# Performance work log

Measured on AMD Instinct MI355X. Metric: run time of the kernel, lower is better.

The kernel has to match this reference:

```python
import jax, jax.numpy as jnp
import numpy as np

BETA = 0.25

def conv1d(x, w, b=None, stride=1, pad=0):
    # x: (B, C_in, T), w: (C_out, C_in, K)
    y = jax.lax.conv_general_dilated(x, w, (stride,), [(pad, pad)],
                                     dimension_numbers=('NCW', 'OIW', 'NCW'))
    if b is not None:
        y = y + b[None, :, None]
    return y

def setup_inputs() -> dict:
    key = jax.random.key(0)
    ks = jax.random.split(key, 16)
    B, C_in, T = 64, 64, 4096
    h, rh, D, K = 128, 64, 64, 512
    s = 0.05
    f32 = jnp.float32
    return {
        'x': jax.random.normal(ks[0], (B, C_in, T), f32),
        'w1': jax.random.normal(ks[1], (h // 2, C_in, 4), f32) * s,
        'b1': jnp.zeros((h // 2,), f32),
        'w2': jax.random.normal(ks[2], (h, h // 2, 4), f32) * s,
        'b2': jnp.zeros((h,), f32),
        'w3': jax.random.normal(ks[3], (h, h, 3), f32) * s,
        'b3': jnp.zeros((h,), f32),
        'res0_w1': jax.random.normal(ks[4], (rh, h, 3), f32) * s,
        'res0_w2': jax.random.normal(ks[5], (h, rh, 1), f32) * s,
        'res1_w1': jax.random.normal(ks[6], (rh, h, 3), f32) * s,
        'res1_w2': jax.random.normal(ks[7], (h, rh, 1), f32) * s,
        'w_out': jax.random.normal(ks[8], (D, h, 1), f32) * s,
        'b_out': jnp.zeros((D,), f32),
        'wpq': jax.random.normal(ks[9], (D, D, 1), f32) * s,
        'bpq': jnp.zeros((D,), f32),
        'codebook': jax.random.uniform(ks[10], (K, D), f32, -1.0 / K, 1.0 / K),
    }

def reference(x, w1, b1, w2, b2, w3, b3, res0_w1, res0_w2, res1_w1, res1_w2,
              w_out, b_out, wpq, bpq, codebook):
    # ---- Encoder (1D conv downsampling + residual stack) ----
    hcur = jax.nn.relu(conv1d(x, w1, b1, stride=2, pad=1))       # (B, h/2, T/2)
    hcur = jax.nn.relu(conv1d(hcur, w2, b2, stride=2, pad=1))    # (B, h, T/4)
    hcur = conv1d(hcur, w3, b3, stride=1, pad=1)                 # (B, h, T')
    for wa, wb in ((res0_w1, res0_w2), (res1_w1, res1_w2)):
        hcur = hcur + conv1d(jax.nn.relu(conv1d(jax.nn.relu(hcur), wa, None, 1, 1)), wb, None, 1, 0)
    hcur = jax.nn.relu(hcur)
    hcur = conv1d(hcur, w_out, b_out)                            # (B, D, T')
    # ---- pre-quantization 1x1 conv (module permutes to channel-first and back) ----
    z = conv1d(hcur, wpq, bpq)                                   # (B, D, T')
    z_e = jnp.transpose(z, (0, 2, 1))                            # (B, T', D)
    B, Tq, D = z_e.shape
    K = codebook.shape[0]
    # ---- Vector quantization ----
    flat = z_e.reshape(-1, D)                                    # (N, D)
    d = (jnp.sum(flat * flat, axis=1, keepdims=True)
         + jnp.sum(codebook * codebook, axis=1)[None, :]
         - 2.0 * flat @ codebook.T)                              # (N, K)
    idx = jnp.argmin(d, axis=1)                                  # (N,)
    encodings = jax.nn.one_hot(idx, K, dtype=z_e.dtype)          # (N, K)
    z_q = codebook[idx].reshape(B, Tq, D)                        # gather
    sg = jax.lax.stop_gradient
    embedding_loss = jnp.mean((sg(z_q) - z_e) ** 2) + BETA * jnp.mean((z_q - sg(z_e)) ** 2)
    z_q_st = z_e + sg(z_q - z_e)                                 # straight-through
    e_mean = jnp.mean(encodings, axis=0)
    perplexity = jnp.exp(-jnp.sum(e_mean * jnp.log(e_mean + 1e-10)))
    encoding_indices = idx.reshape(-1, 1)
    return (embedding_loss, z_q_st, perplexity, z_e, encodings, encoding_indices)
```

## Files before the change

### kernel.cpp

```cpp
#include <hip/hip_runtime.h>
#include <math.h>


typedef short short8 __attribute__((ext_vector_type(8)));
typedef float f32x4 __attribute__((ext_vector_type(4)));

__device__ __forceinline__ unsigned short bf16hi(float f) {
  unsigned u = __builtin_bit_cast(unsigned, f);
  return (unsigned short)((u + 0x7FFFu + ((u >> 16) & 1u)) >> 16);
}
__device__ __forceinline__ float bf16tof(unsigned short h) {
  unsigned u = ((unsigned)h) << 16;
  return __builtin_bit_cast(float, u);
}
__device__ __forceinline__ void split3(float f, unsigned short& h,
                                       unsigned short& m, unsigned short& l) {
  h = bf16hi(f);
  float r = f - bf16tof(h);
  m = bf16hi(r);
  l = bf16hi(r - bf16tof(m));
}

template<int CIN, int TAPS, int S, bool RELU_IN, bool HAS_BIAS, bool RESID,
         bool CHW_IN, bool OUT_NOGUARD>
__global__ __launch_bounds__(256) void conv_mfma(
    const float* __restrict__ in, const short* __restrict__ Ab,
    const float* __restrict__ bias, const float* __restrict__ resid,
    float* __restrict__ out, int Tin, int Tout, int MTG)
{
  constexpr int nCk   = CIN / 32;
  constexpr int RS    = (S == 2) ? 130 : ((TAPS == 3) ? 66 : 64);
  constexpr int ROWBS = 40;

  __shared__ short xhi[RS * ROWBS];
  __shared__ short xmd[RS * ROWBS];
  __shared__ short xlo[RS * ROWBS];

  const int tid  = threadIdx.x;
  const int lane = tid & 63;
  const int wv   = tid >> 6;
  const int ih   = wv & 1;
  const int jh   = wv >> 1;
  const int tl   = lane & 15;
  const int q    = lane >> 4;
  const int b    = blockIdx.y;
  const int t0   = blockIdx.x * 64;
  const int co0  = blockIdx.z * 64;
  const int COUT = MTG * 16;

  const int rbase = (S == 2) ? (2 * t0) : ((TAPS == 3) ? t0 : (t0 + 1));

  f32x4 acc[2][2] = {};

  for (int ch = 0; ch < nCk; ch++) {
    if (ch) __syncthreads();

    if constexpr (!CHW_IN) {
      for (int i = tid; i < RS * 8; i += 256) {
        int rl = i >> 3;
        int c4 = (i & 7) * 4;
        int rg = rbase + rl;
        const float* sp = in + ((size_t)b * (Tin + 2) + rg) * CIN + ch * 32 + c4;
        float4 v = *(const float4*)sp;
        if (RELU_IN) {
          v.x = fmaxf(v.x, 0.f); v.y = fmaxf(v.y, 0.f);
          v.z = fmaxf(v.z, 0.f); v.w = fmaxf(v.w, 0.f);
        }
        float vv[4] = {v.x, v.y, v.z, v.w};
        unsigned short h[4], m[4], l[4];
        #pragma unroll
        for (int e = 0; e < 4; e++) split3(vv[e], h[e], m[e], l[e]);
        int slot = (S == 2) ? ((rl & 1) * 65 + (rl >> 1)) : rl;
        int off = slot * ROWBS + c4;
        uint2 uh, um, ul;
        uh.x = (unsigned)h[0] | ((unsigned)h[1] << 16);
        uh.y = (unsigned)h[2] | ((unsigned)h[3] << 16);
        um.x = (unsigned)m[0] | ((unsigned)m[1] << 16);
        um.y = (unsigned)m[2] | ((unsigned)m[3] << 16);
        ul.x = (unsigned)l[0] | ((unsigned)l[1] << 16);
        ul.y = (unsigned)l[2] | ((unsigned)l[3] << 16);
        *(uint2*)(xhi + off) = uh;
        *(uint2*)(xmd + off) = um;
        *(uint2*)(xlo + off) = ul;
      }
    } else {
      if (tid < 32) {
        int cig = ch * 32 + tid;
        int tin = 2 * t0 - 1;
        float v = 0.f;
        if (tin >= 0) v = in[((size_t)b * 64 + cig) * Tin + tin];
        unsigned short h, m, l;
        split3(v, h, m, l);
        xhi[tid] = (short)h;
        xmd[tid] = (short)m;
        xlo[tid] = (short)l;
      }
      int cil = tid >> 3, tq = tid & 7;
      for (int base = tq * 4; base <= 128; base += 32) {
        int tin0 = 2 * t0 + base;
        const float* sp = in + ((size_t)b * 64 + ch * 32 + cil) * Tin + tin0;
        float vv[4];
        if (tin0 + 3 < Tin) {
          float4 t4 = *(const float4*)sp;
          vv[0] = t4.x; vv[1] = t4.y; vv[2] = t4.z; vv[3] = t4.w;
        } else {
          #pragma unroll
          for (int e = 0; e < 4; e++) vv[e] = (tin0 + e < Tin) ? sp[e] : 0.f;
        }
        #pragma unroll
        for (int e = 0; e < 4; e++) {
          int rl = base + e + 1;
          if (rl <= 129) {
            unsigned short h, m, l;
            split3(vv[e], h, m, l);
            int slot = (rl & 1) * 65 + (rl >> 1);
            xhi[slot * ROWBS + cil] = (short)h;
            xmd[slot * ROWBS + cil] = (short)m;
            xlo[slot * ROWBS + cil] = (short)l;
          }
        }
      }
    }
    __syncthreads();

    #pragma unroll
    for (int tap = 0; tap < TAPS; tap++) {
      short8 ah[2], am[2], al[2];
      #pragma unroll
      for (int mi = 0; mi < 2; mi++) {
        const short* ab = Ab +
            (size_t)(((ch * TAPS + tap) * MTG + (co0 >> 4) + ih * 2 + mi) * 3) * 512
            + lane * 8;
        ah[mi] = *(const short8*)ab;
        am[mi] = *(const short8*)(ab + 512);
        al[mi] = *(const short8*)(ab + 1024);
      }
      #pragma unroll
      for (int nt = 0; nt < 2; nt++) {
        int tpos = jh * 32 + nt * 16 + tl;
        int slot;
        if constexpr (S == 2)         slot = (tap & 1) * 65 + tpos + (tap >> 1);
        else if constexpr (TAPS == 3) slot = tpos + tap;
        else                          slot = tpos;
        const int xo = slot * ROWBS + q * 8;
        short8 bh = *(const short8*)(xhi + xo);
        short8 bm = *(const short8*)(xmd + xo);
        short8 bl = *(const short8*)(xlo + xo);
        #pragma unroll
        for (int mi = 0; mi < 2; mi++) {
          acc[mi][nt] = __builtin_amdgcn_mfma_f32_16x16x32_bf16(ah[mi], bh, acc[mi][nt], 0, 0, 0);
          acc[mi][nt] = __builtin_amdgcn_mfma_f32_16x16x32_bf16(ah[mi], bm, acc[mi][nt], 0, 0, 0);
          acc[mi][nt] = __builtin_amdgcn_mfma_f32_16x16x32_bf16(am[mi], bh, acc[mi][nt], 0, 0, 0);
          acc[mi][nt] = __builtin_amdgcn_mfma_f32_16x16x32_bf16(am[mi], bm, acc[mi][nt], 0, 0, 0);
          acc[mi][nt] = __builtin_amdgcn_mfma_f32_16x16x32_bf16(ah[mi], bl, acc[mi][nt], 0, 0, 0);
          acc[mi][nt] = __builtin_amdgcn_mfma_f32_16x16x32_bf16(al[mi], bh, acc[mi][nt], 0, 0, 0);
        }
      }
    }
  }

  #pragma unroll
  for (int mi = 0; mi < 2; mi++) {
    #pragma unroll
    for (int nt = 0; nt < 2; nt++) {
      int t  = t0 + jh * 32 + nt * 16 + tl;
      int co = co0 + (ih * 2 + mi) * 16 + q * 4;
      f32x4 a = acc[mi][nt];
      float4 v = {a[0], a[1], a[2], a[3]};
      if constexpr (HAS_BIAS) {
        float4 bb = *(const float4*)(bias + co);
        v.x += bb.x; v.y += bb.y; v.z += bb.z; v.w += bb.w;
      }
      if constexpr (RESID) {
        float4 rr = *(const float4*)(resid + ((size_t)b * (Tout + 2) + t + 1) * COUT + co);
        v.x += rr.x; v.y += rr.y; v.z += rr.z; v.w += rr.w;
      }
      float* op;
      if constexpr (OUT_NOGUARD) op = out + ((size_t)b * Tout + t) * COUT + co;
      else                       op = out + ((size_t)b * (Tout + 2) + t + 1) * COUT + co;
      *(float4*)op = v;
    }
  }
}

__global__ __launch_bounds__(256) void prep_small(
    const float* __restrict__ wout, const float* __restrict__ bout,
    const float* __restrict__ wpq, const float* __restrict__ bpq,
    const float* __restrict__ cb,
    float* __restrict__ Wc, float* __restrict__ bc, float* __restrict__ cnorm)
{
  const int tid = threadIdx.x;
  for (int i = tid; i < 64 * 128; i += 256) {
    int d = i >> 7, c = i & 127;
    float s = 0.f;
    for (int e = 0; e < 64; e++) s = fmaf(wpq[d * 64 + e], wout[e * 128 + c], s);
    Wc[i] = s;
  }
  for (int i = tid; i < 64; i += 256) {
    float s = bpq[i];
    for (int e = 0; e < 64; e++) s = fmaf(wpq[i * 64 + e], bout[e], s);
    bc[i] = s;
  }
  for (int k = tid; k < 512; k += 256) {
    float s = 0.f;
    for (int d = 0; d < 64; d++) { float c = cb[k * 64 + d]; s = fmaf(c, c, s); }
    cnorm[k] = s;
  }
}

__device__ __forceinline__ void buildA(const float* w, short* dst,
                                       int COUT, int CIN, int TAPS, int idx)
{
  int lane = idx & 63;
  int rest = idx >> 6;
  int hl   = rest % 3;  rest /= 3;
  int mtg  = rest % (COUT / 16); rest /= (COUT / 16);
  int tap  = rest % TAPS;
  int chunk = rest / TAPS;
  int co  = mtg * 16 + (lane & 15);
  int ci0 = chunk * 32 + (lane >> 4) * 8;
  short v[8];
  #pragma unroll
  for (int j = 0; j < 8; j++) {
    float f = w[((size_t)co * CIN + ci0 + j) * TAPS + tap];
    unsigned short h, m, l;
    h = bf16hi(f);
    float r = f - bf16tof(h);
    m = bf16hi(r);
    l = bf16hi(r - bf16tof(m));
    v[j] = (hl == 0) ? (short)h : ((hl == 1) ? (short)m : (short)l);
  }
  int MTG = COUT / 16;
  size_t o = ((((size_t)(chunk * TAPS + tap) * MTG + mtg) * 3 + hl) * 64 + lane) * 8;
  #pragma unroll
  for (int j = 0; j < 8; j++) dst[o + j] = v[j];
}

__global__ __launch_bounds__(256) void prep_w_all(
    const float* w1, const float* w2, const float* w3,
    const float* r0a, const float* r0b, const float* r1a, const float* r1b,
    const float* Wc,
    short* A1, short* A2, short* A3, short* A4, short* A5, short* A6,
    short* A7, short* A8)
{
  int g = blockIdx.x * 256 + threadIdx.x;
  if      (g < 6144)  buildA(w1,  A1, 64,  64,  4, g);
  else if (g < 18432) buildA(w2,  A2, 128, 64,  4, g - 6144);
  else if (g < 36864) buildA(w3,  A3, 128, 128, 3, g - 18432);
  else if (g < 46080) buildA(r0a, A4, 64,  128, 3, g - 36864);
  else if (g < 49152) buildA(r0b, A5, 128, 64,  1, g - 46080);
  else if (g < 58368) buildA(r1a, A6, 64,  128, 3, g - 49152);
  else if (g < 61440) buildA(r1b, A7, 128, 64,  1, g - 58368);
  else if (g < 64512) buildA(Wc,  A8, 64,  128, 1, g - 61440);
}

__global__ __launch_bounds__(256) void zero_guards(
    float* __restrict__ sA, float* __restrict__ sB1,
    float* __restrict__ sB2, float* __restrict__ sC)
{
  int gt = blockIdx.x * 256 + threadIdx.x;
  int NT = gridDim.x * 256;
  for (int i = gt; i < 64 * 2 * 64; i += NT) {
    int b = i >> 7, r = (i >> 6) & 1, c = i & 63;
    sA[((size_t)b * 2050 + r * 2049) * 64 + c] = 0.f;
  }
  for (int i = gt; i < 64 * 2 * 128; i += NT) {
    int b = i >> 8, r = (i >> 7) & 1, c = i & 127;
    size_t o = ((size_t)b * 1026 + r * 1025) * 128 + c;
    sB1[o] = 0.f; sB2[o] = 0.f;
  }
  for (int i = gt; i < 64 * 2 * 64; i += NT) {
    int b = i >> 7, r = (i >> 6) & 1, c = i & 63;
    sC[((size_t)b * 1026 + r * 1025) * 64 + c] = 0.f;
  }
}

__global__ __launch_bounds__(256) void vq_k(
    const float* __restrict__ ze, const float* __restrict__ cb,
    const float* __restrict__ cnorm,
    float* __restrict__ zq_out, float* __restrict__ enc,
    float* __restrict__ idx_out,
    int* __restrict__ counts, float* __restrict__ loss_accum)
{
  __shared__ float rv0[256], rv1[256];
  __shared__ int   ri0[256], ri1[256];
  __shared__ int   idx_s[128];
  __shared__ float ls[4];

  const int tid  = threadIdx.x;
  const int lane = tid & 63;
  const int wv   = tid >> 6;
  const int wvu  = __builtin_amdgcn_readfirstlane(wv);
  const int n0   = blockIdx.x * 128;

  float zr0[64], zr1[64];
  {
    const float* zp0 = ze + (size_t)(n0 + lane) * 64;
    const float* zp1 = ze + (size_t)(n0 + 64 + lane) * 64;
    #pragma unroll
    for (int j = 0; j < 32; j++) {
      float2 a = *(const float2*)(zp0 + 2 * j);
      float2 b = *(const float2*)(zp1 + 2 * j);
      zr0[2 * j] = a.x; zr0[2 * j + 1] = a.y;
      zr1[2 * j] = b.x; zr1[2 * j + 1] = b.y;
    }
  }

  float best0 = 3.4e38f, best1 = 3.4e38f;
  int   bi0 = 0, bi1 = 0;

  #pragma unroll 2
  for (int r = 0; r < 128; r++) {
    const int c = wvu * 128 + r;
    const float* crow = cb + (size_t)c * 64;
    float s00 = 0.f, s01 = 0.f, s02 = 0.f, s03 = 0.f;
    float s10 = 0.f, s11 = 0.f, s12 = 0.f, s13 = 0.f;
    #pragma unroll
    for (int d = 0; d < 64; d += 4) {
      float4 cv = *(const float4*)(crow + d);
      s00 = fmaf(cv.x, zr0[d],     s00);
      s01 = fmaf(cv.y, zr0[d + 1], s01);
      s02 = fmaf(cv.z, zr0[d + 2], s02);
      s03 = fmaf(cv.w, zr0[d + 3], s03);
      s10 = fmaf(cv.x, zr1[d],     s10);
      s11 = fmaf(cv.y, zr1[d + 1], s11);
      s12 = fmaf(cv.z, zr1[d + 2], s12);
      s13 = fmaf(cv.w, zr1[d + 3], s13);
    }
    float cn = cnorm[c];
    float d0 = cn - 2.f * ((s00 + s01) + (s02 + s03));
    float d1 = cn - 2.f * ((s10 + s11) + (s12 + s13));
    if (d0 < best0) { best0 = d0; bi0 = c; }
    if (d1 < best1) { best1 = d1; bi1 = c; }
  }

  rv0[wv * 64 + lane] = best0; ri0[wv * 64 + lane] = bi0;
  rv1[wv * 64 + lane] = best1; ri1[wv * 64 + lane] = bi1;
  __syncthreads();
  if (wv == 0) {
    float bv = rv0[lane]; int bi = ri0[lane];
    #pragma unroll
    for (int w = 1; w < 4; w++) {
      float v = rv0[w * 64 + lane]; int i2 = ri0[w * 64 + lane];
      if (v < bv || (v == bv && i2 < bi)) { bv = v; bi = i2; }
    }
    idx_s[lane] = bi;
    idx_out[n0 + lane] = (float)bi;
    atomicAdd(&counts[bi], 1);
  } else if (wv == 1) {
    float bv = rv1[lane]; int bi = ri1[lane];
    #pragma unroll
    for (int w = 1; w < 4; w++) {
      float v = rv1[w * 64 + lane]; int i2 = ri1[w * 64 + lane];
      if (v < bv || (v == bv && i2 < bi)) { bv = v; bi = i2; }
    }
    idx_s[64 + lane] = bi;
    idx_out[n0 + 64 + lane] = (float)bi;
    atomicAdd(&counts[bi], 1);
  }
  __syncthreads();

  float lsum = 0.f;
  const size_t obase = (size_t)n0 * 64;
  #pragma unroll
  for (int j = 0; j < 32; j++) {
    int pos = j * 256 + tid;
    int p = pos >> 6, d = pos & 63;
    int id = idx_s[p];
    float zq  = cb[id * 64 + d];
    float zev = ze[obase + pos];
    float df  = zq - zev;
    lsum = fmaf(df, df, lsum);
    zq_out[obase + pos] = zq;
  }
  #pragma unroll
  for (int off = 32; off; off >>= 1) lsum += __shfl_down(lsum, off, 64);
  if (lane == 0) ls[wv] = lsum;

  for (int pp = 0; pp < 128; pp += 2) {
    int p   = pp + (tid >> 7);
    int col = (tid & 127) * 4;
    int id  = idx_s[p];
    float4 v;
    v.x = (col     == id) ? 1.0f : 0.0f;
    v.y = (col + 1 == id) ? 1.0f : 0.0f;
    v.z = (col + 2 == id) ? 1.0f : 0.0f;
    v.w = (col + 3 == id) ? 1.0f : 0.0f;
    *(float4*)(enc + (size_t)(n0 + p) * 512 + col) = v;
  }

  __syncthreads();
  if (tid == 0) atomicAdd(loss_accum, ls[0] + ls[1] + ls[2] + ls[3]);
}

__global__ __launch_bounds__(256) void fin_k(
    const int* __restrict__ counts, const float* __restrict__ loss_accum,
    float* __restrict__ loss_out, float* __restrict__ perp_out)
{
  __shared__ float sd[256];
  const int tid = threadIdx.x;
  float h = 0.f;
  for (int k = tid; k < 512; k += 256) {
    float em = (float)counts[k] * (1.0f / 65536.0f);
    h += em * logf(em + 1e-10f);
  }
  sd[tid] = h;
  __syncthreads();
  for (int s = 128; s; s >>= 1) {
    if (tid < s) sd[tid] += sd[tid + s];
    __syncthreads();
  }
  if (tid == 0) {
    *perp_out = expf(-sd[0]);
    *loss_out = *loss_accum * 1.25f / 4194304.f;
  }
}

extern "C" void kernel_launch(void* const* d_in, const int* in_sizes, int n_in,
                              void* d_out, int out_size, void* d_ws, size_t ws_size,
                              hipStream_t stream)
{
  const float* x    = (const float*)d_in[0];
  const float* w1   = (const float*)d_in[1];
  const float* b1   = (const float*)d_in[2];
  const float* w2   = (const float*)d_in[3];
  const float* b2   = (const float*)d_in[4];
  const float* w3   = (const float*)d_in[5];
  const float* b3   = (const float*)d_in[6];
  const float* r0a  = (const float*)d_in[7];
  const float* r0b  = (const float*)d_in[8];
  const float* r1a  = (const float*)d_in[9];
  const float* r1b  = (const float*)d_in[10];
  const float* wout = (const float*)d_in[11];
  const float* bout = (const float*)d_in[12];
  const float* wpq  = (const float*)d_in[13];
  const float* bpq  = (const float*)d_in[14];
  const float* cb   = (const float*)d_in[15];

  float* out = (float*)d_out;
  float* f   = (float*)d_ws;

  float* slotA  = f;
  float* slotB1 = f + 8396800;
  float* slotB2 = f + 16801792;
  float* slotC  = f + 25206784;
  float* Wcf    = f + 29409280;
  float* bc     = f + 29417472;
  float* cnorm  = f + 29417536;
  int*   counts = (int*)(f + 29418048);
  float* lossa  = f + 29418560;
  short* AB     = (short*)(f + 29418576);
  short* A1 = AB;
  short* A2 = AB + 49152;
  short* A3 = AB + 147456;
  short* A4 = AB + 294912;
  short* A5 = AB + 368640;
  short* A6 = AB + 393216;
  short* A7 = AB + 466944;
  short* A8 = AB + 491520;

  float* loss_out = out;
  float* zq_out   = out + 1;
  float* perp_out = out + 4194305;
  float* ze_out   = out + 4194306;
  float* enc_out  = out + 8388610;
  float* idx_out  = out + 41943042;

  prep_small<<<dim3(1), dim3(256), 0, stream>>>(wout, bout, wpq, bpq, cb,
                                                Wcf, bc, cnorm);
  prep_w_all<<<dim3(252), dim3(256), 0, stream>>>(w1, w2, w3, r0a, r0b, r1a,
                                                  r1b, Wcf,
                                                  A1, A2, A3, A4, A5, A6, A7, A8);
  zero_guards<<<dim3(32), dim3(256), 0, stream>>>(slotA, slotB1, slotB2, slotC);
  hipMemsetAsync(counts, 0, 2052, stream);

  conv_mfma<64, 4, 2, false, true, false, true, false>
      <<<dim3(32, 64, 1), dim3(256), 0, stream>>>(x, A1, b1, nullptr, slotA,
                                                  4096, 2048, 4);
  conv_mfma<64, 4, 2, true, true, false, false, false>
      <<<dim3(16, 64, 2), dim3(256), 0, stream>>>(slotA, A2, b2, nullptr, slotB1,
                                                  2048, 1024, 8);
  conv_mfma<128, 3, 1, true, true, false, false, false>
      <<<dim3(16, 64, 2), dim3(256), 0, stream>>>(slotB1, A3, b3, nullptr, slotB2,
                                                  1024, 1024, 8);
  conv_mfma<128, 3, 1, true, false, false, false, false>
      <<<dim3(16, 64, 1), dim3(256), 0, stream>>>(slotB2, A4, nullptr, nullptr,
                                                  slotC, 1024, 1024, 4);
  conv_mfma<64, 1, 1, true, false, true, false, false>
      <<<dim3(16, 64, 2), dim3(256), 0, stream>>>(slotC, A5, nullptr, slotB2,
                                                  slotB1, 1024, 1024, 8);
  conv_mfma<128, 3, 1, true, false, false, false, false>
      <<<dim3(16, 64, 1), dim3(256), 0, stream>>>(slotB1, A6, nullptr, nullptr,
                                                  slotC, 1024, 1024, 4);
  conv_mfma<64, 1, 1, true, false, true, false, false>
      <<<dim3(16, 64, 2), dim3(256), 0, stream>>>(slotC, A7, nullptr, slotB1,
                                                  slotB2, 1024, 1024, 8);
  conv_mfma<128, 1, 1, true, true, false, false, true>
      <<<dim3(16, 64, 1), dim3(256), 0, stream>>>(slotB2, A8, bc, nullptr,
                                                  ze_out, 1024, 1024, 4);

  vq_k<<<dim3(512), dim3(256), 0, stream>>>(ze_out, cb, cnorm, zq_out, enc_out,
                                            idx_out, counts, lossa);
  fin_k<<<dim3(1), dim3(256), 0, stream>>>(counts, lossa, loss_out, perp_out);
}
```

Baseline: 739.3 us.

## Compute VQ codebook distances with split-bf16 MFMA instead of scalar FMA

The VQ distance search now runs on matrix cores. The codebook is pre-split into three bf16 pieces in MFMA fragment layout inside the weight-prep kernel. z_e tiles are split the same way and staged in LDS, and six partial products approximate the fp32 dot product. The code keeps a score of -0.5*||c||^2 + z·c and takes its argmax, which replaces the per-wave scalar FMA loops and the LDS cross-wave reduction with lane shuffles. The risk is small precision differences that could flip argmin ties against the fp32 reference.

```diff
diff --git a/kernel.cpp b/kernel.cpp
--- a/kernel.cpp
+++ b/kernel.cpp
@@ -187,7 +187,7 @@
     const float* __restrict__ wout, const float* __restrict__ bout,
     const float* __restrict__ wpq, const float* __restrict__ bpq,
     const float* __restrict__ cb,
-    float* __restrict__ Wc, float* __restrict__ bc, float* __restrict__ cnorm)
+    float* __restrict__ Wc, float* __restrict__ bc, float* __restrict__ cnormd)
 {
   const int tid = threadIdx.x;
   for (int i = tid; i < 64 * 128; i += 256) {
@@ -204,7 +204,7 @@
   for (int k = tid; k < 512; k += 256) {
     float s = 0.f;
     for (int d = 0; d < 64; d++) { float c = cb[k * 64 + d]; s = fmaf(c, c, s); }
-    cnorm[k] = s;
+    cnormd[k] = -0.5f * s;
   }
 }
 
@@ -224,24 +224,41 @@
   for (int j = 0; j < 8; j++) {
     float f = w[((size_t)co * CIN + ci0 + j) * TAPS + tap];
     unsigned short h, m, l;
-    h = bf16hi(f);
-    float r = f - bf16tof(h);
-    m = bf16hi(r);
-    l = bf16hi(r - bf16tof(m));
+    split3(f, h, m, l);
     v[j] = (hl == 0) ? (short)h : ((hl == 1) ? (short)m : (short)l);
   }
   int MTG = COUT / 16;
   size_t o = ((((size_t)(chunk * TAPS + tap) * MTG + mtg) * 3 + hl) * 64 + lane) * 8;
   #pragma unroll
   for (int j = 0; j < 8; j++) dst[o + j] = v[j];
+}
+
+__device__ __forceinline__ void buildAcb(const float* cb, short* dst, int g)
+{
+  int lane = g & 63;
+  int rest = g >> 6;
+  int s  = rest % 3; rest /= 3;
+  int kc = rest & 1;
+  int ct = rest >> 1;
+  int tl = lane & 15, q = lane >> 4;
+  int code = ct * 16 + tl;
+  int k0 = kc * 32 + q * 8;
+  size_t o = (((size_t)(ct * 2 + kc) * 3 + s) * 64 + lane) * 8;
+  #pragma unroll
+  for (int j = 0; j < 8; j++) {
+    float f = cb[(size_t)code * 64 + k0 + j];
+    unsigned short h, m, l;
+    split3(f, h, m, l);
+    dst[o + j] = (s == 0) ? (short)h : ((s == 1) ? (short)m : (short)l);
+  }
 }
 
 __global__ __launch_bounds__(256) void prep_w_all(
     const float* w1, const float* w2, const float* w3,
     const float* r0a, const float* r0b, const float* r1a, const float* r1b,
-    const float* Wc,
+    const float* Wc, const float* cb,
     short* A1, short* A2, short* A3, short* A4, short* A5, short* A6,
-    short* A7, short* A8)
+    short* A7, short* A8, short* Acb)
 {
   int g = blockIdx.x * 256 + threadIdx.x;
   if      (g < 6144)  buildA(w1,  A1, 64,  64,  4, g);
@@ -252,6 +269,7 @@
   else if (g < 58368) buildA(r1a, A6, 64,  128, 3, g - 49152);
   else if (g < 61440) buildA(r1b, A7, 128, 64,  1, g - 58368);
   else if (g < 64512) buildA(Wc,  A8, 64,  128, 1, g - 61440);
+  else if (g < 76800) buildAcb(cb, Acb, g - 64512);
 }
 
 __global__ __launch_bounds__(256) void zero_guards(
@@ -277,86 +295,115 @@
 
 __global__ __launch_bounds__(256) void vq_k(
     const float* __restrict__ ze, const float* __restrict__ cb,
-    const float* __restrict__ cnorm,
+    const float* __restrict__ cnormd, const short* __restrict__ Acb,
     float* __restrict__ zq_out, float* __restrict__ enc,
     float* __restrict__ idx_out,
     int* __restrict__ counts, float* __restrict__ loss_accum)
 {
-  __shared__ float rv0[256], rv1[256];
-  __shared__ int   ri0[256], ri1[256];
+  __shared__ short zh[128 * 72];
+  __shared__ short zm[128 * 72];
+  __shared__ short zl[128 * 72];
   __shared__ int   idx_s[128];
   __shared__ float ls[4];
 
   const int tid  = threadIdx.x;
   const int lane = tid & 63;
   const int wv   = tid >> 6;
-  const int wvu  = __builtin_amdgcn_readfirstlane(wv);
+  const int tl   = lane & 15;
+  const int q    = lane >> 4;
   const int n0   = blockIdx.x * 128;
 
-  float zr0[64], zr1[64];
   {
-    const float* zp0 = ze + (size_t)(n0 + lane) * 64;
-    const float* zp1 = ze + (size_t)(n0 + 64 + lane) * 64;
+    const float* zb = ze + (size_t)n0 * 64;
     #pragma unroll
-    for (int j = 0; j < 32; j++) {
-      float2 a = *(const float2*)(zp0 + 2 * j);
-      float2 b = *(const float2*)(zp1 + 2 * j);
-      zr0[2 * j] = a.x; zr0[2 * j + 1] = a.y;
-      zr1[2 * j] = b.x; zr1[2 * j + 1] = b.y;
-    }
-  }
-
-  float best0 = 3.4e38f, best1 = 3.4e38f;
+    for (int j = 0; j < 8; j++) {
+      int off = j * 1024 + tid * 4;
+      int p = off >> 6, d = off & 63;
+      float2 v0 = *(const float2*)(zb + off);
+      float2 v1 = *(const float2*)(zb + off + 2);
+      float vv[4] = {v0.x, v0.y, v1.x, v1.y};
+      unsigned short h[4], m[4], l[4];
+      #pragma unroll
+      for (int e = 0; e < 4; e++) split3(vv[e], h[e], m[e], l[e]);
+      int o = p * 72 + d;
+      uint2 uh, um, ul;
+      uh.x = (unsigned)h[0] | ((unsigned)h[1] << 16);
+      uh.y = (unsigned)h[2] | ((unsigned)h[3] << 16);
+      um.x = (unsigned)m[0] | ((unsigned)m[1] << 16);
+      um.y = (unsigned)m[2] | ((unsigned)m[3] << 16);
+      ul.x = (unsigned)l[0] | ((unsigned)l[1] << 16);
+      ul.y = (unsigned)l[2] | ((unsigned)l[3] << 16);
+      *(uint2*)(zh + o) = uh;
+      *(uint2*)(zm + o) = um;
+      *(uint2*)(zl + o) = ul;
+    }
+  }
+  __syncthreads();
+
+  short8 bh[2][2], bm[2][2], bl[2][2];
+  #pragma unroll
+  for (int pt = 0; pt < 2; pt++) {
+    int row = wv * 32 + pt * 16 + tl;
+    #pragma unroll
+    for (int kc = 0; kc < 2; kc++) {
+      int o = row * 72 + kc * 32 + q * 8;
+      bh[pt][kc] = *(const short8*)(zh + o);
+      bm[pt][kc] = *(const short8*)(zm + o);
+      bl[pt][kc] = *(const short8*)(zl + o);
+    }
+  }
+
+  float best0 = -3.4e38f, best1 = -3.4e38f;
   int   bi0 = 0, bi1 = 0;
 
-  #pragma unroll 2
-  for (int r = 0; r < 128; r++) {
-    const int c = wvu * 128 + r;
-    const float* crow = cb + (size_t)c * 64;
-    float s00 = 0.f, s01 = 0.f, s02 = 0.f, s03 = 0.f;
-    float s10 = 0.f, s11 = 0.f, s12 = 0.f, s13 = 0.f;
+  for (int ct = 0; ct < 32; ct++) {
+    float4 cv = *(const float4*)(cnormd + ct * 16 + q * 4);
+    f32x4 a0 = {cv.x, cv.y, cv.z, cv.w};
+    f32x4 a1 = a0;
     #pragma unroll
-    for (int d = 0; d < 64; d += 4) {
-      float4 cv = *(const float4*)(crow + d);
-      s00 = fmaf(cv.x, zr0[d],     s00);
-      s01 = fmaf(cv.y, zr0[d + 1], s01);
-      s02 = fmaf(cv.z, zr0[d + 2], s02);
-      s03 = fmaf(cv.w, zr0[d + 3], s03);
-      s10 = fmaf(cv.x, zr1[d],     s10);
-      s11 = fmaf(cv.y, zr1[d + 1], s11);
-      s12 = fmaf(cv.z, zr1[d + 2], s12);
-      s13 = fmaf(cv.w, zr1[d + 3], s13);
-    }
-    float cn = cnorm[c];
-    float d0 = cn - 2.f * ((s00 + s01) + (s02 + s03));
-    float d1 = cn - 2.f * ((s10 + s11) + (s12 + s13));
-    if (d0 < best0) { best0 = d0; bi0 = c; }
-    if (d1 < best1) { best1 = d1; bi1 = c; }
-  }
-
-  rv0[wv * 64 + lane] = best0; ri0[wv * 64 + lane] = bi0;
-  rv1[wv * 64 + lane] = best1; ri1[wv * 64 + lane] = bi1;
-  __syncthreads();
-  if (wv == 0) {
-    float bv = rv0[lane]; int bi = ri0[lane];
+    for (int kc = 0; kc < 2; kc++) {
+      const short* ap = Acb + (size_t)((ct * 2 + kc) * 3) * 512 + lane * 8;
+      short8 ah = *(const short8*)ap;
+      short8 am = *(const short8*)(ap + 512);
+      short8 al = *(const short8*)(ap + 1024);
+      a0 = __builtin_amdgcn_mfma_f32_16x16x32_bf16(ah, bh[0][kc], a0, 0, 0, 0);
+      a1 = __builtin_amdgcn_mfma_f32_16x16x32_bf16(ah, bh[1][kc], a1, 0, 0, 0);
+      a0 = __builtin_amdgcn_mfma_f32_16x16x32_bf16(ah, bm[0][kc], a0, 0, 0, 0);
+      a1 = __builtin_amdgcn_mfma_f32_16x16x32_bf16(ah, bm[1][kc], a1, 0, 0, 0);
+      a0 = __builtin_amdgcn_mfma_f32_16x16x32_bf16(am, bh[0][kc], a0, 0, 0, 0);
+      a1 = __builtin_amdgcn_mfma_f32_16x16x32_bf16(am, bh[1][kc], a1, 0, 0, 0);
+      a0 = __builtin_amdgcn_mfma_f32_16x16x32_bf16(am, bm[0][kc], a0, 0, 0, 0);
+      a1 = __builtin_amdgcn_mfma_f32_16x16x32_bf16(am, bm[1][kc], a1, 0, 0, 0);
+      a0 = __builtin_amdgcn_mfma_f32_16x16x32_bf16(ah, bl[0][kc], a0, 0, 0, 0);
+      a1 = __builtin_amdgcn_mfma_f32_16x16x32_bf16(ah, bl[1][kc], a1, 0, 0, 0);
+      a0 = __builtin_amdgcn_mfma_f32_16x16x32_bf16(al, bh[0][kc], a0, 0, 0, 0);
+      a1 = __builtin_amdgcn_mfma_f32_16x16x32_bf16(al, bh[1][kc], a1, 0, 0, 0);
+    }
     #pragma unroll
-    for (int w = 1; w < 4; w++) {
-      float v = rv0[w * 64 + lane]; int i2 = ri0[w * 64 + lane];
-      if (v < bv || (v == bv && i2 < bi)) { bv = v; bi = i2; }
-    }
-    idx_s[lane] = bi;
-    idx_out[n0 + lane] = (float)bi;
-    atomicAdd(&counts[bi], 1);
-  } else if (wv == 1) {
-    float bv = rv1[lane]; int bi = ri1[lane];
-    #pragma unroll
-    for (int w = 1; w < 4; w++) {
-      float v = rv1[w * 64 + lane]; int i2 = ri1[w * 64 + lane];
-      if (v < bv || (v == bv && i2 < bi)) { bv = v; bi = i2; }
-    }
-    idx_s[64 + lane] = bi;
-    idx_out[n0 + 64 + lane] = (float)bi;
-    atomicAdd(&counts[bi], 1);
+    for (int r = 0; r < 4; r++) {
+      int code = ct * 16 + q * 4 + r;
+      float v0 = a0[r], v1 = a1[r];
+      if (v0 > best0) { best0 = v0; bi0 = code; }
+      if (v1 > best1) { best1 = v1; bi1 = code; }
+    }
+  }
+
+  #pragma unroll
+  for (int mask = 16; mask <= 32; mask <<= 1) {
+    float v0 = __shfl_xor(best0, mask, 64); int i0 = __shfl_xor(bi0, mask, 64);
+    float v1 = __shfl_xor(best1, mask, 64); int i1 = __shfl_xor(bi1, mask, 64);
+    if (v0 > best0 || (v0 == best0 && i0 < bi0)) { best0 = v0; bi0 = i0; }
+    if (v1 > best1 || (v1 == best1 && i1 < bi1)) { best1 = v1; bi1 = i1; }
+  }
+  if (q == 0) {
+    int p0 = wv * 32 + tl;
+    int p1 = p0 + 16;
+    idx_s[p0] = bi0;
+    idx_s[p1] = bi1;
+    idx_out[n0 + p0] = (float)bi0;
+    idx_out[n0 + p1] = (float)bi1;
+    atomicAdd(&counts[bi0], 1);
+    atomicAdd(&counts[bi1], 1);
   }
   __syncthreads();
 
@@ -446,7 +493,7 @@
   float* slotC  = f + 25206784;
   float* Wcf    = f + 29409280;
   float* bc     = f + 29417472;
-  float* cnorm  = f + 29417536;
+  float* cnormd = f + 29417536;
   int*   counts = (int*)(f + 29418048);
   float* lossa  = f + 29418560;
   short* AB     = (short*)(f + 29418576);
@@ -458,6 +505,7 @@
   short* A6 = AB + 393216;
   short* A7 = AB + 466944;
   short* A8 = AB + 491520;
+  short* Acb = (short*)(f + 29676624);
 
   float* loss_out = out;
   float* zq_out   = out + 1;
@@ -467,10 +515,11 @@
   float* idx_out  = out + 41943042;
 
   prep_small<<<dim3(1), dim3(256), 0, stream>>>(wout, bout, wpq, bpq, cb,
-                                                Wcf, bc, cnorm);
-  prep_w_all<<<dim3(252), dim3(256), 0, stream>>>(w1, w2, w3, r0a, r0b, r1a,
-                                                  r1b, Wcf,
-                                                  A1, A2, A3, A4, A5, A6, A7, A8);
+                                                Wcf, bc, cnormd);
+  prep_w_all<<<dim3(300), dim3(256), 0, stream>>>(w1, w2, w3, r0a, r0b, r1a,
+                                                  r1b, Wcf, cb,
+                                                  A1, A2, A3, A4, A5, A6, A7,
+                                                  A8, Acb);
   zero_guards<<<dim3(32), dim3(256), 0, stream>>>(slotA, slotB1, slotB2, slotC);
   hipMemsetAsync(counts, 0, 2052, stream);
 
@@ -499,7 +548,7 @@
       <<<dim3(16, 64, 1), dim3(256), 0, stream>>>(slotB2, A8, bc, nullptr,
                                                   ze_out, 1024, 1024, 4);
 
-  vq_k<<<dim3(512), dim3(256), 0, stream>>>(ze_out, cb, cnorm, zq_out, enc_out,
-                                            idx_out, counts, lossa);
+  vq_k<<<dim3(512), dim3(256), 0, stream>>>(ze_out, cb, cnormd, Acb, zq_out,
+                                            enc_out, idx_out, counts, lossa);
   fin_k<<<dim3(1), dim3(256), 0, stream>>>(counts, lossa, loss_out, perp_out);
 }
```

New measurement: 698.2 us. 1.06x faster.
